# Kernel tuning notes

Measured on AMD Instinct MI355X. Metric: run time of the kernel, lower is better.

The kernel has to match this reference:

```python
import jax, jax.numpy as jnp
import numpy as np

D_MODEL, H, D_FF = 1024, 16, 4096
B, S = 2, 2048
EPS = 1e-05


def layer_norm(x, gamma, beta):
    # Matches torch: mean and UNBIASED std over last dim, scalar gamma/beta,
    # and eps added to std (not variance).
    mean = jnp.mean(x, axis=-1, keepdims=True)
    var = jnp.sum((x - mean) ** 2, axis=-1, keepdims=True) / (x.shape[-1] - 1)
    return gamma * (x - mean) / (jnp.sqrt(var) + EPS) + beta


def setup_inputs() -> dict:
    key = jax.random.key(0)
    ks = jax.random.split(key, 16)
    sd = 1.0 / np.sqrt(D_MODEL)
    sf = 1.0 / np.sqrt(D_FF)
    return {
        "x": jax.random.normal(ks[0], (B, S, D_MODEL), jnp.float32),
        "mask": jnp.ones((1, 1, S, S), jnp.int32),
        "wq": jax.random.uniform(ks[1], (D_MODEL, D_MODEL), jnp.float32, -sd, sd),
        "bq": jax.random.uniform(ks[2], (D_MODEL,), jnp.float32, -sd, sd),
        "wk": jax.random.uniform(ks[3], (D_MODEL, D_MODEL), jnp.float32, -sd, sd),
        "bk": jax.random.uniform(ks[4], (D_MODEL,), jnp.float32, -sd, sd),
        "wv": jax.random.uniform(ks[5], (D_MODEL, D_MODEL), jnp.float32, -sd, sd),
        "bv": jax.random.uniform(ks[6], (D_MODEL,), jnp.float32, -sd, sd),
        "wo": jax.random.uniform(ks[7], (D_MODEL, D_MODEL), jnp.float32, -sd, sd),
        "bo": jax.random.uniform(ks[8], (D_MODEL,), jnp.float32, -sd, sd),
        "w1": jax.random.uniform(ks[9], (D_FF, D_MODEL), jnp.float32, -sd, sd),
        "b1": jax.random.uniform(ks[10], (D_FF,), jnp.float32, -sd, sd),
        "w2": jax.random.uniform(ks[11], (D_MODEL, D_FF), jnp.float32, -sf, sf),
        "b2": jax.random.uniform(ks[12], (D_MODEL,), jnp.float32, -sf, sf),
        "gamma1": jnp.ones((1,), jnp.float32),
        "beta1": jnp.zeros((1,), jnp.float32),
        "gamma2": jnp.ones((1,), jnp.float32),
        "beta2": jnp.zeros((1,), jnp.float32),
    }


def reference(x, mask, wq, bq, wk, bk, wv, bv, wo, bo, w1, b1, w2, b2,
              gamma1, beta1, gamma2, beta2):
    d_k = D_MODEL // H

    # --- residual 1: pre-LN self-attention ---
    xn = layer_norm(x, gamma1, beta1)
    q = (xn @ wq.T + bq).reshape(B, S, H, d_k).transpose(0, 2, 1, 3)
    k = (xn @ wk.T + bk).reshape(B, S, H, d_k).transpose(0, 2, 1, 3)
    v = (xn @ wv.T + bv).reshape(B, S, H, d_k).transpose(0, 2, 1, 3)

    scores = jnp.einsum("bhqd,bhkd->bhqk", q, k) / jnp.sqrt(
        jnp.asarray(d_k, x.dtype))
    scores = jnp.where(mask == 0, jnp.asarray(-1e9, x.dtype), scores)
    attn = jax.nn.softmax(scores, axis=-1)
    ctx = jnp.einsum("bhqk,bhkd->bhqd", attn, v)
    ctx = ctx.transpose(0, 2, 1, 3).reshape(B, S, D_MODEL)
    x = x + (ctx @ wo.T + bo)

    # --- residual 2: pre-LN feed-forward ---
    xn = layer_norm(x, gamma2, beta2)
    h = jax.nn.relu(xn @ w1.T + b1)
    x = x + (h @ w2.T + b2)
    return x
```

## Files before the change

### kernel.cpp

```cpp
#include <hip/hip_runtime.h>


typedef __bf16 bf16_t;
typedef __attribute__((ext_vector_type(8))) __bf16 bf16x8;
typedef __attribute__((ext_vector_type(4))) __bf16 bf16x4;
typedef __attribute__((ext_vector_type(2))) __bf16 bf16x2;
typedef __attribute__((ext_vector_type(4))) float f32x4;
typedef __attribute__((ext_vector_type(16))) float f32x16;
typedef __attribute__((ext_vector_type(2))) unsigned uint32x2;
typedef __attribute__((ext_vector_type(4))) unsigned uint32x4;

#define MB (1024ull * 1024ull)
#define QSCALE 0.18033688011112043f

__device__ __forceinline__ void gload_lds16(const bf16_t* g, bf16_t* l) {
    __builtin_amdgcn_global_load_lds(
        (const __attribute__((address_space(1))) void*)g,
        (__attribute__((address_space(3))) void*)l, 16, 0, 0);
}

__device__ __forceinline__ int bswz(int row) { return ((row >> 1) & 3) << 3; }

__device__ __forceinline__ int swz(int row, int col) {
    return row * 64 + ((((col >> 3) ^ row) & 7) << 3) + (col & 7);
}

__device__ __forceinline__ unsigned cvtpk(float a, float b) {
    bf16x2 v = {(__bf16)a, (__bf16)b};
    return __builtin_bit_cast(unsigned, v);
}

__global__ __launch_bounds__(256) void cvt_all(
    const float* __restrict__ wq, const float* __restrict__ wk,
    const float* __restrict__ wv, const float* __restrict__ wo,
    const float* __restrict__ w1, const float* __restrict__ w2,
    bf16_t* __restrict__ wqkv, bf16_t* __restrict__ wob, bf16_t* __restrict__ w1b,
    bf16_t* __restrict__ w2b) {
    const int b = blockIdx.x, t = threadIdx.x;
    const float* in;
    bf16_t* out;
    int i;
    if (b < 1024) { in = wq; out = wqkv; i = b * 256 + t; }
    else if (b < 2048) { in = wk; out = wqkv + 1048576; i = (b - 1024) * 256 + t; }
    else if (b < 3072) { in = wv; out = wqkv + 2097152; i = (b - 2048) * 256 + t; }
    else if (b < 4096) { in = wo; out = wob; i = (b - 3072) * 256 + t; }
    else if (b < 8192) { in = w1; out = w1b; i = (b - 4096) * 256 + t; }
    else { in = w2; out = w2b; i = (b - 8192) * 256 + t; }
    float4 v = ((const float4*)in)[i];
    bf16x4 o = {(__bf16)v.x, (__bf16)v.y, (__bf16)v.z, (__bf16)v.w};
    ((bf16x4*)out)[i] = o;
}

__global__ __launch_bounds__(256) void ln_kernel(const float* __restrict__ x,
                                                 bf16_t* __restrict__ out,
                                                 const float* __restrict__ gamma,
                                                 const float* __restrict__ beta) {
    const int lane = threadIdx.x & 63;
    const int row = blockIdx.x * 4 + (threadIdx.x >> 6);
    const float* xr = x + (size_t)row * 1024;
    float4 v[4];
    float s = 0.f;
#pragma unroll
    for (int i = 0; i < 4; ++i) {
        v[i] = ((const float4*)xr)[i * 64 + lane];
        s += v[i].x + v[i].y + v[i].z + v[i].w;
    }
#pragma unroll
    for (int o = 32; o; o >>= 1) s += __shfl_xor(s, o);
    float mean = s * (1.f / 1024.f);
    float vs = 0.f;
#pragma unroll
    for (int i = 0; i < 4; ++i) {
        float a = v[i].x - mean, b = v[i].y - mean, c = v[i].z - mean, d = v[i].w - mean;
        vs += a * a + b * b + c * c + d * d;
    }
#pragma unroll
    for (int o = 32; o; o >>= 1) vs += __shfl_xor(vs, o);
    float inv = 1.f / (sqrtf(vs * (1.f / 1023.f)) + 1e-5f);
    float g = gamma[0] * inv, bb = beta[0];
    bf16_t* orow = out + (size_t)row * 1024;
#pragma unroll
    for (int i = 0; i < 4; ++i) {
        bf16x4 ov = {(__bf16)((v[i].x - mean) * g + bb), (__bf16)((v[i].y - mean) * g + bb),
                     (__bf16)((v[i].z - mean) * g + bb), (__bf16)((v[i].w - mean) * g + bb)};
        *(bf16x4*)(orow + (i * 64 + lane) * 4) = ov;
    }
}

template <int KERN>
__global__ __launch_bounds__(512, 2) void gemm256(
    const bf16_t* __restrict__ A, const bf16_t* __restrict__ Bw, int K,
    const float* __restrict__ bias0, const float* __restrict__ bias1,
    const float* __restrict__ bias2, void* __restrict__ o0, void* __restrict__ o1,
    void* __restrict__ o2) {
    __shared__ bf16_t L[4 * 16384];
    const int t = threadIdx.x, lane = t & 63, w = t >> 6;
    const int wm = w >> 2, wn = w & 3;
    const int l15 = lane & 15, l4 = lane >> 4;
    const int bm = blockIdx.x, bn = blockIdx.y;
    const int NT = K >> 5;
    const bf16_t* Ab = A + (size_t)bm * 256 * K;
    const bf16_t* Bb = Bw + (size_t)bn * 256 * K;
    const int srow = t >> 2, pcol = (t & 3) * 8;
    f32x4 acc[8][4] = {};

    auto stageA = [&](int tt) {
        bf16_t* s = L + (tt & 3) * 16384;
        const int kb = tt * 32;
#pragma unroll
        for (int i = 0; i < 2; ++i) {
            int row = i * 128 + srow;
            int lcol = pcol ^ bswz(row);
            gload_lds16(Ab + (size_t)row * K + kb + lcol, s + i * 4096 + t * 8);
        }
    };
    auto stageB = [&](int tt) {
        bf16_t* s = L + (tt & 3) * 16384 + 8192;
        const int kb = tt * 32;
#pragma unroll
        for (int i = 0; i < 2; ++i) {
            int row = i * 128 + srow;
            int lcol = pcol ^ bswz(row);
            gload_lds16(Bb + (size_t)row * K + kb + lcol, s + i * 4096 + t * 8);
        }
    };

    stageA(0); stageB(0); stageA(1); stageB(1); stageA(2); stageB(2);
    asm volatile("s_waitcnt vmcnt(8)" ::: "memory");
    __builtin_amdgcn_s_barrier();

    for (int tt = 0; tt < NT; ++tt) {
        bf16_t* s = L + (tt & 3) * 16384;
        bf16_t* sB = s + 8192;
        bf16x8 af[4], bfr[4];
#pragma unroll
        for (int m = 0; m < 4; ++m) {
            int row = wm * 128 + m * 16 + l15;
            af[m] = *(const bf16x8*)(s + row * 32 + ((l4 * 8) ^ bswz(row)));
        }
#pragma unroll
        for (int n = 0; n < 4; ++n) {
            int row = wn * 64 + n * 16 + l15;
            bfr[n] = *(const bf16x8*)(sB + row * 32 + ((l4 * 8) ^ bswz(row)));
        }
        if (tt + 3 < NT) stageA(tt + 3);
        __builtin_amdgcn_s_barrier();
        __builtin_amdgcn_s_setprio(1);
#pragma unroll
        for (int m = 0; m < 4; ++m)
#pragma unroll
            for (int n = 0; n < 4; ++n)
                acc[m][n] = __builtin_amdgcn_mfma_f32_16x16x32_bf16(af[m], bfr[n], acc[m][n],
                                                                   0, 0, 0);
        __builtin_amdgcn_s_setprio(0);
        __builtin_amdgcn_s_barrier();
#pragma unroll
        for (int m = 0; m < 4; ++m) {
            int row = wm * 128 + 64 + m * 16 + l15;
            af[m] = *(const bf16x8*)(s + row * 32 + ((l4 * 8) ^ bswz(row)));
        }
        if (tt + 3 < NT) stageB(tt + 3);
        __builtin_amdgcn_s_barrier();
        __builtin_amdgcn_s_setprio(1);
#pragma unroll
        for (int m = 0; m < 4; ++m)
#pragma unroll
            for (int n = 0; n < 4; ++n)
                acc[4 + m][n] = __builtin_amdgcn_mfma_f32_16x16x32_bf16(af[m], bfr[n],
                                                                       acc[4 + m][n], 0, 0, 0);
        __builtin_amdgcn_s_setprio(0);
        if (tt + 3 < NT)
            asm volatile("s_waitcnt vmcnt(8)" ::: "memory");
        else if (tt + 2 < NT)
            asm volatile("s_waitcnt vmcnt(4)" ::: "memory");
        else
            asm volatile("s_waitcnt vmcnt(0)" ::: "memory");
        __builtin_amdgcn_s_barrier();
    }

    if (KERN == 1) {
        const int colb = bn * 256 + wn * 64;
        float bb[4];
#pragma unroll
        for (int n = 0; n < 4; ++n) bb[n] = bias0[colb + n * 16 + l15];
#pragma unroll
        for (int m = 0; m < 8; ++m) {
            const int row0 = bm * 256 + wm * 128 + m * 16 + (l4 << 2);
#pragma unroll
            for (int n = 0; n < 4; ++n)
#pragma unroll
                for (int j = 0; j < 4; ++j) {
                    float v = acc[m][n][j] + bb[n];
                    ((bf16_t*)o0)[(size_t)(row0 + j) * 4096 + colb + n * 16 + l15] =
                        (bf16_t)(v > 0.f ? v : 0.f);
                }
        }
        return;
    }
    if (bn < 8) {
        const bool isq = bn < 4;
        const float* bias = isq ? bias0 : bias1;
        const int head = (bn & 3) * 4 + wn;
        const int b = (bm * 256) >> 11;
        const int srow0 = (bm * 256 + wm * 128) & 2047;
        bf16_t* dst = (bf16_t*)(isq ? o0 : o1) + ((size_t)(b * 16 + head) << 17);
        float bb[4];
#pragma unroll
        for (int n = 0; n < 4; ++n) bb[n] = bias[head * 64 + n * 16 + l15];
#pragma unroll
        for (int m = 0; m < 8; ++m)
#pragma unroll
            for (int n = 0; n < 4; ++n)
#pragma unroll
                for (int j = 0; j < 4; ++j) {
                    int srw = srow0 + m * 16 + (l4 << 2) + j;
                    float v = acc[m][n][j] + bb[n];
                    if (isq) v *= QSCALE;
                    dst[((size_t)srw << 6) + n * 16 + l15] = (bf16_t)v;
                }
    } else {
        const int head = (bn - 8) * 4 + wn;
        const int b = (bm * 256) >> 11;
        const int sbase = (bm * 256 + wm * 128) & 2047;
        bf16_t* P = L + w * 8192;
        float bb[4];
#pragma unroll
        for (int n = 0; n < 4; ++n) bb[n] = bias2[head * 64 + n * 16 + l15];
#pragma unroll
        for (int m = 0; m < 8; ++m)
#pragma unroll
            for (int n = 0; n < 4; ++n) {
                int d = n * 16 + l15;
                int sl = m * 16 + (l4 << 2);
                bf16x4 pk = {(__bf16)(acc[m][n][0] + bb[n]), (__bf16)(acc[m][n][1] + bb[n]),
                             (__bf16)(acc[m][n][2] + bb[n]), (__bf16)(acc[m][n][3] + bb[n])};
                *(bf16x4*)(P + d * 128 + (sl ^ ((d & 7) << 3))) = pk;
            }
#pragma unroll
        for (int p = 0; p < 16; ++p) {
            int id = p * 64 + lane;
            int d = id >> 4, c8 = (id & 15) * 8;
            bf16x8 vv = *(const bf16x8*)(P + d * 128 + (c8 ^ ((d & 7) << 3)));
            *(bf16x8*)((bf16_t*)o2 + (((size_t)(b * 16 + head) * 64 + d) << 11) + sbase + c8) =
                vv;
        }
    }
}

__global__ __launch_bounds__(256, 2) void gemm128sq(
    const bf16_t* __restrict__ A, const bf16_t* __restrict__ Bw, int K,
    const float* __restrict__ bias, const float* __restrict__ resid,
    float* __restrict__ out) {
    __shared__ bf16_t L[4 * 8192];
    const int t = threadIdx.x, lane = t & 63, w = t >> 6;
    const int wr = w >> 1, wc = w & 1;
    const int l15 = lane & 15, l4 = lane >> 4;
    const int bm = blockIdx.x, bn = blockIdx.y;
    const int NT = K >> 5;
    const bf16_t* Ab = A + (size_t)bm * 128 * K;
    const bf16_t* Bb = Bw + (size_t)bn * 128 * K;
    const int srow = t >> 2, pcol = (t & 3) * 8;
    f32x4 acc[4][4] = {};

    auto STAGE = [&](int tt) {
        bf16_t* s = L + (tt & 3) * 8192;
        const int kb = tt * 32;
#pragma unroll
        for (int i = 0; i < 2; ++i) {
            int row = i * 64 + srow;
            int lcol = pcol ^ bswz(row);
            gload_lds16(Ab + (size_t)row * K + kb + lcol, s + i * 2048 + t * 8);
            gload_lds16(Bb + (size_t)row * K + kb + lcol, s + 4096 + i * 2048 + t * 8);
        }
    };

    STAGE(0); STAGE(1); STAGE(2);
    asm volatile("s_waitcnt vmcnt(8)" ::: "memory");
    __builtin_amdgcn_s_barrier();

    for (int tt = 0; tt < NT; ++tt) {
        bf16_t* s = L + (tt & 3) * 8192;
        bf16x8 af[4], bfr[4];
#pragma unroll
        for (int m = 0; m < 4; ++m) {
            int row = wr * 64 + m * 16 + l15;
            af[m] = *(const bf16x8*)(s + row * 32 + ((l4 * 8) ^ bswz(row)));
        }
#pragma unroll
        for (int n = 0; n < 4; ++n) {
            int row = wc * 64 + n * 16 + l15;
            bfr[n] = *(const bf16x8*)(s + 4096 + row * 32 + ((l4 * 8) ^ bswz(row)));
        }
        if (tt + 3 < NT) STAGE(tt + 3);
        __builtin_amdgcn_s_barrier();
        __builtin_amdgcn_s_setprio(1);
#pragma unroll
        for (int m = 0; m < 4; ++m)
#pragma unroll
            for (int n = 0; n < 4; ++n)
                acc[m][n] = __builtin_amdgcn_mfma_f32_16x16x32_bf16(af[m], bfr[n], acc[m][n],
                                                                   0, 0, 0);
        __builtin_amdgcn_s_setprio(0);
        if (tt + 3 < NT)
            asm volatile("s_waitcnt vmcnt(8)" ::: "memory");
        else if (tt + 2 < NT)
            asm volatile("s_waitcnt vmcnt(4)" ::: "memory");
        else
            asm volatile("s_waitcnt vmcnt(0)" ::: "memory");
        __builtin_amdgcn_s_barrier();
    }

#pragma unroll
    for (int m = 0; m < 4; ++m) {
        const int row0 = bm * 128 + wr * 64 + m * 16 + (l4 << 2);
#pragma unroll
        for (int n = 0; n < 4; ++n) {
            const int col = bn * 128 + wc * 64 + n * 16 + l15;
#pragma unroll
            for (int j = 0; j < 4; ++j) {
                const int row = row0 + j;
                out[(size_t)row * 1024 + col] =
                    resid[(size_t)row * 1024 + col] + acc[m][n][j] + bias[col];
            }
        }
    }
}

__global__ __launch_bounds__(256, 2) void attn_kernel(const bf16_t* __restrict__ q,
                                                      const bf16_t* __restrict__ k,
                                                      const bf16_t* __restrict__ vt,
                                                      bf16_t* __restrict__ ctx) {
    __shared__ bf16_t Kl[64 * 64];
    __shared__ bf16_t Vl[64 * 64];
    const int t = threadIdx.x, lane = t & 63, w = t >> 6;
    const int bh = blockIdx.y;
    const bf16_t* qg = q + (size_t)bh * 2048 * 64;
    const bf16_t* kg = k + (size_t)bh * 2048 * 64;
    const bf16_t* vg = vt + (size_t)bh * 64 * 2048;
    const int r = t >> 3, c8 = (t & 7) * 8;
    const int l31 = lane & 31, h = lane >> 5;
    const int qrow = blockIdx.x * 128 + w * 32 + l31;

    bf16x8 qf[4];
#pragma unroll
    for (int kd = 0; kd < 4; ++kd)
        qf[kd] = *(const bf16x8*)(qg + (size_t)qrow * 64 + kd * 16 + h * 8);

    f32x16 o0 = {}, o1 = {};
    float mi = -1e30f, li = 0.f;

    {
        bf16x8 k0 = *(const bf16x8*)(kg + (size_t)r * 64 + c8);
        bf16x8 k1 = *(const bf16x8*)(kg + (size_t)(r + 32) * 64 + c8);
        bf16x8 v0 = *(const bf16x8*)(vg + (size_t)r * 2048 + c8);
        bf16x8 v1 = *(const bf16x8*)(vg + (size_t)(r + 32) * 2048 + c8);
        *(bf16x8*)(Kl + swz(r, c8)) = k0;
        *(bf16x8*)(Kl + swz(r + 32, c8)) = k1;
        *(bf16x8*)(Vl + swz(r, c8)) = v0;
        *(bf16x8*)(Vl + swz(r + 32, c8)) = v1;
    }

    for (int kt = 0; kt < 2048; kt += 64) {
        __syncthreads();
        bf16x8 k0, k1, v0, v1;
        const bool more = (kt + 64) < 2048;
        if (more) {
            k0 = *(const bf16x8*)(kg + (size_t)(kt + 64 + r) * 64 + c8);
            k1 = *(const bf16x8*)(kg + (size_t)(kt + 64 + r + 32) * 64 + c8);
            v0 = *(const bf16x8*)(vg + (size_t)r * 2048 + kt + 64 + c8);
            v1 = *(const bf16x8*)(vg + (size_t)(r + 32) * 2048 + kt + 64 + c8);
        }
        f32x16 sT0 = {}, sT1 = {};
        __builtin_amdgcn_s_setprio(1);
#pragma unroll
        for (int kd = 0; kd < 4; ++kd) {
            bf16x8 ka0 = *(const bf16x8*)(Kl + swz(l31, kd * 16 + h * 8));
            bf16x8 ka1 = *(const bf16x8*)(Kl + swz(32 + l31, kd * 16 + h * 8));
            sT0 = __builtin_amdgcn_mfma_f32_32x32x16_bf16(ka0, qf[kd], sT0, 0, 0, 0);
            sT1 = __builtin_amdgcn_mfma_f32_32x32x16_bf16(ka1, qf[kd], sT1, 0, 0, 0);
        }
        __builtin_amdgcn_s_setprio(0);
        float mx = fmaxf(sT0[0], sT0[1]);
#pragma unroll
        for (int i = 2; i < 16; ++i) mx = fmaxf(mx, sT0[i]);
#pragma unroll
        for (int i = 0; i < 16; ++i) mx = fmaxf(mx, sT1[i]);
        mx = fmaxf(mx, __shfl_xor(mx, 32));
        if (!__all(mx <= mi + 8.f)) {
            float mn = fmaxf(mi, mx);
            float al = __builtin_amdgcn_exp2f(mi - mn);
            mi = mn;
            li *= al;
            o0 *= al;
            o1 *= al;
        }
        f32x16 e0, e1;
        float rs = 0.f;
#pragma unroll
        for (int i = 0; i < 16; ++i) {
            e0[i] = __builtin_amdgcn_exp2f(sT0[i] - mi);
            rs += e0[i];
        }
#pragma unroll
        for (int i = 0; i < 16; ++i) {
            e1[i] = __builtin_amdgcn_exp2f(sT1[i] - mi);
            rs += e1[i];
        }
        rs += __shfl_xor(rs, 32);
        li += rs;
        bf16x8 pa[4];
#pragma unroll
        for (int kd = 0; kd < 4; ++kd) {
            const f32x16& e = (kd < 2) ? e0 : e1;
            const int R0l = 8 * (kd & 1);
            const int R0h = R0l + 4;
            unsigned U0 = cvtpk(e[R0l + 0], e[R0l + 1]);
            unsigned V0 = cvtpk(e[R0l + 2], e[R0l + 3]);
            unsigned U1 = cvtpk(e[R0h + 0], e[R0h + 1]);
            unsigned V1 = cvtpk(e[R0h + 2], e[R0h + 3]);
            uint32x2 ru = __builtin_amdgcn_permlane32_swap(U0, U1, false, false);
            uint32x2 rv = __builtin_amdgcn_permlane32_swap(V0, V1, false, false);
            uint32x4 pw = {ru.x, rv.x, ru.y, rv.y};
            pa[kd] = __builtin_bit_cast(bf16x8, pw);
        }
        __builtin_amdgcn_s_setprio(1);
#pragma unroll
        for (int kd = 0; kd < 4; ++kd) {
            bf16x8 va0 = *(const bf16x8*)(Vl + swz(l31, kd * 16 + h * 8));
            bf16x8 va1 = *(const bf16x8*)(Vl + swz(32 + l31, kd * 16 + h * 8));
            o0 = __builtin_amdgcn_mfma_f32_32x32x16_bf16(va0, pa[kd], o0, 0, 0, 0);
            o1 = __builtin_amdgcn_mfma_f32_32x32x16_bf16(va1, pa[kd], o1, 0, 0, 0);
        }
        __builtin_amdgcn_s_setprio(0);
        __syncthreads();
        if (more) {
            *(bf16x8*)(Kl + swz(r, c8)) = k0;
            *(bf16x8*)(Kl + swz(r + 32, c8)) = k1;
            *(bf16x8*)(Vl + swz(r, c8)) = v0;
            *(bf16x8*)(Vl + swz(r + 32, c8)) = v1;
        }
    }
    float inv = 1.f / li;
    size_t base = ((size_t)(bh >> 4) * 2048 + qrow) * 1024 + (bh & 15) * 64;
#pragma unroll
    for (int g = 0; g < 4; ++g) {
        bf16x4 ov0 = {(__bf16)(o0[4 * g + 0] * inv), (__bf16)(o0[4 * g + 1] * inv),
                      (__bf16)(o0[4 * g + 2] * inv), (__bf16)(o0[4 * g + 3] * inv)};
        *(bf16x4*)(ctx + base + 8 * g + 4 * h) = ov0;
        bf16x4 ov1 = {(__bf16)(o1[4 * g + 0] * inv), (__bf16)(o1[4 * g + 1] * inv),
                      (__bf16)(o1[4 * g + 2] * inv), (__bf16)(o1[4 * g + 3] * inv)};
        *(bf16x4*)(ctx + base + 32 + 8 * g + 4 * h) = ov1;
    }
}

extern "C" void kernel_launch(void* const* d_in, const int* in_sizes, int n_in,
                              void* d_out, int out_size, void* d_ws, size_t ws_size,
                              hipStream_t stream) {
    const float* x = (const float*)d_in[0];
    const float* wq = (const float*)d_in[2];
    const float* bq = (const float*)d_in[3];
    const float* wk = (const float*)d_in[4];
    const float* bk = (const float*)d_in[5];
    const float* wv = (const float*)d_in[6];
    const float* bv = (const float*)d_in[7];
    const float* wo = (const float*)d_in[8];
    const float* bo = (const float*)d_in[9];
    const float* w1 = (const float*)d_in[10];
    const float* b1 = (const float*)d_in[11];
    const float* w2 = (const float*)d_in[12];
    const float* b2 = (const float*)d_in[13];
    const float* gamma1 = (const float*)d_in[14];
    const float* beta1 = (const float*)d_in[15];
    const float* gamma2 = (const float*)d_in[16];
    const float* beta2 = (const float*)d_in[17];

    char* ws = (char*)d_ws;
    bf16_t* wqkv = (bf16_t*)(ws + 0);
    bf16_t* wob = (bf16_t*)(ws + 6 * MB);
    bf16_t* w1b = (bf16_t*)(ws + 8 * MB);
    bf16_t* w2b = (bf16_t*)(ws + 16 * MB);
    bf16_t* xnb = (bf16_t*)(ws + 24 * MB);
    bf16_t* qb = (bf16_t*)(ws + 32 * MB);
    bf16_t* kb = (bf16_t*)(ws + 40 * MB);
    bf16_t* vtb = (bf16_t*)(ws + 48 * MB);
    bf16_t* ctxb = (bf16_t*)(ws + 56 * MB);
    float* x1 = (float*)(ws + 64 * MB);
    bf16_t* hb = (bf16_t*)(ws + 32 * MB);

    cvt_all<<<12288, 256, 0, stream>>>(wq, wk, wv, wo, w1, w2, wqkv, wob, w1b, w2b);

    ln_kernel<<<1024, 256, 0, stream>>>(x, xnb, gamma1, beta1);
    gemm256<0><<<dim3(16, 12), 512, 0, stream>>>(xnb, wqkv, 1024, bq, bk, bv, qb, kb, vtb);
    attn_kernel<<<dim3(16, 32), 256, 0, stream>>>(qb, kb, vtb, ctxb);
    gemm128sq<<<dim3(32, 8), 256, 0, stream>>>(ctxb, wob, 1024, bo, x, x1);
    ln_kernel<<<1024, 256, 0, stream>>>(x1, xnb, gamma2, beta2);
    gemm256<1><<<dim3(16, 16), 512, 0, stream>>>(xnb, w1b, 1024, b1, nullptr, nullptr, hb,
                                                 nullptr, nullptr);
    gemm128sq<<<dim3(32, 8), 256, 0, stream>>>(hb, w2b, 4096, b2, x1, (float*)d_out);
}
```

Measured before the change: 212.5 us.

## Split-K the FFN down-projection and remap attention blocks onto XCDs

The FFN2 GEMM (K=4096) gets split into two K halves over blockIdx.z. This doubles the grid from 256 to 512 blocks to fill the GPU better. Each half writes bf16 partials, and a new combine kernel adds the partials, the residual and the bias. The attention grid is flattened to 1D, with block ids remapped so that blocks sharing a batch-head land on the same XCD for L2 reuse of K/V. The split adds an extra kernel launch and partial-buffer traffic, and rounding the partials to bf16 costs some precision.

```diff
diff --git a/kernel.cpp b/kernel.cpp
--- a/kernel.cpp
+++ b/kernel.cpp
@@ -247,18 +247,20 @@
     }
 }
 
+template <int SPLIT>
 __global__ __launch_bounds__(256, 2) void gemm128sq(
-    const bf16_t* __restrict__ A, const bf16_t* __restrict__ Bw, int K,
+    const bf16_t* __restrict__ A, const bf16_t* __restrict__ Bw, int stride, int Ks,
     const float* __restrict__ bias, const float* __restrict__ resid,
-    float* __restrict__ out) {
+    void* __restrict__ o0, void* __restrict__ o1) {
     __shared__ bf16_t L[4 * 8192];
     const int t = threadIdx.x, lane = t & 63, w = t >> 6;
     const int wr = w >> 1, wc = w & 1;
     const int l15 = lane & 15, l4 = lane >> 4;
     const int bm = blockIdx.x, bn = blockIdx.y;
-    const int NT = K >> 5;
-    const bf16_t* Ab = A + (size_t)bm * 128 * K;
-    const bf16_t* Bb = Bw + (size_t)bn * 128 * K;
+    const int NT = Ks >> 5;
+    const size_t kofs = SPLIT ? (size_t)blockIdx.z * Ks : 0;
+    const bf16_t* Ab = A + (size_t)bm * 128 * stride + kofs;
+    const bf16_t* Bb = Bw + (size_t)bn * 128 * stride + kofs;
     const int srow = t >> 2, pcol = (t & 3) * 8;
     f32x4 acc[4][4] = {};
 
@@ -269,8 +271,8 @@
         for (int i = 0; i < 2; ++i) {
             int row = i * 64 + srow;
             int lcol = pcol ^ bswz(row);
-            gload_lds16(Ab + (size_t)row * K + kb + lcol, s + i * 2048 + t * 8);
-            gload_lds16(Bb + (size_t)row * K + kb + lcol, s + 4096 + i * 2048 + t * 8);
+            gload_lds16(Ab + (size_t)row * stride + kb + lcol, s + i * 2048 + t * 8);
+            gload_lds16(Bb + (size_t)row * stride + kb + lcol, s + 4096 + i * 2048 + t * 8);
         }
     };
 
@@ -319,11 +321,33 @@
 #pragma unroll
             for (int j = 0; j < 4; ++j) {
                 const int row = row0 + j;
-                out[(size_t)row * 1024 + col] =
-                    resid[(size_t)row * 1024 + col] + acc[m][n][j] + bias[col];
+                if (SPLIT == 0) {
+                    ((float*)o0)[(size_t)row * 1024 + col] =
+                        resid[(size_t)row * 1024 + col] + acc[m][n][j] + bias[col];
+                } else {
+                    bf16_t* po = (bf16_t*)(blockIdx.z ? o1 : o0);
+                    po[(size_t)row * 1024 + col] = (bf16_t)acc[m][n][j];
+                }
             }
         }
     }
+}
+
+__global__ __launch_bounds__(256) void ffn2_combine(
+    const bf16_t* __restrict__ p0, const bf16_t* __restrict__ p1,
+    const float* __restrict__ resid, const float* __restrict__ bias,
+    float* __restrict__ out) {
+    int i = blockIdx.x * 256 + threadIdx.x;
+    float4 r = ((const float4*)resid)[i];
+    bf16x4 a = ((const bf16x4*)p0)[i];
+    bf16x4 b = ((const bf16x4*)p1)[i];
+    float4 bs = ((const float4*)bias)[i & 255];
+    float4 o;
+    o.x = r.x + (float)a.x + (float)b.x + bs.x;
+    o.y = r.y + (float)a.y + (float)b.y + bs.y;
+    o.z = r.z + (float)a.z + (float)b.z + bs.z;
+    o.w = r.w + (float)a.w + (float)b.w + bs.w;
+    ((float4*)out)[i] = o;
 }
 
 __global__ __launch_bounds__(256, 2) void attn_kernel(const bf16_t* __restrict__ q,
@@ -333,13 +357,16 @@
     __shared__ bf16_t Kl[64 * 64];
     __shared__ bf16_t Vl[64 * 64];
     const int t = threadIdx.x, lane = t & 63, w = t >> 6;
-    const int bh = blockIdx.y;
+    const int bid = blockIdx.x;
+    const int xcd = bid & 7, j = bid >> 3;
+    const int bh = xcd + ((j >> 4) << 3);
+    const int qx = j & 15;
     const bf16_t* qg = q + (size_t)bh * 2048 * 64;
     const bf16_t* kg = k + (size_t)bh * 2048 * 64;
     const bf16_t* vg = vt + (size_t)bh * 64 * 2048;
     const int r = t >> 3, c8 = (t & 7) * 8;
     const int l31 = lane & 31, h = lane >> 5;
-    const int qrow = blockIdx.x * 128 + w * 32 + l31;
+    const int qrow = qx * 128 + w * 32 + l31;
 
     bf16x8 qf[4];
 #pragma unroll
@@ -486,15 +513,19 @@
     bf16_t* ctxb = (bf16_t*)(ws + 56 * MB);
     float* x1 = (float*)(ws + 64 * MB);
     bf16_t* hb = (bf16_t*)(ws + 32 * MB);
+    bf16_t* p0 = (bf16_t*)(ws + 0);
+    bf16_t* p1 = (bf16_t*)(ws + 24 * MB);
 
     cvt_all<<<12288, 256, 0, stream>>>(wq, wk, wv, wo, w1, w2, wqkv, wob, w1b, w2b);
 
     ln_kernel<<<1024, 256, 0, stream>>>(x, xnb, gamma1, beta1);
     gemm256<0><<<dim3(16, 12), 512, 0, stream>>>(xnb, wqkv, 1024, bq, bk, bv, qb, kb, vtb);
-    attn_kernel<<<dim3(16, 32), 256, 0, stream>>>(qb, kb, vtb, ctxb);
-    gemm128sq<<<dim3(32, 8), 256, 0, stream>>>(ctxb, wob, 1024, bo, x, x1);
+    attn_kernel<<<512, 256, 0, stream>>>(qb, kb, vtb, ctxb);
+    gemm128sq<0><<<dim3(32, 8), 256, 0, stream>>>(ctxb, wob, 1024, 1024, bo, x, x1, nullptr);
     ln_kernel<<<1024, 256, 0, stream>>>(x1, xnb, gamma2, beta2);
     gemm256<1><<<dim3(16, 16), 512, 0, stream>>>(xnb, w1b, 1024, b1, nullptr, nullptr, hb,
                                                  nullptr, nullptr);
-    gemm128sq<<<dim3(32, 8), 256, 0, stream>>>(hb, w2b, 4096, b2, x1, (float*)d_out);
-}
+    gemm128sq<1><<<dim3(32, 8, 2), 256, 0, stream>>>(hb, w2b, 4096, 2048, nullptr, nullptr,
+                                                     p0, p1);
+    ffn2_combine<<<4096, 256, 0, stream>>>(p0, p1, x1, b2, (float*)d_out);
+}
```

Result: no change. 212.4 us (-0.0%).
